# Optimization experiments

Hardware: AMD Instinct MI355X
Metric: run time of the kernel (lower is better)

Reference implementation:

```python
import jax, jax.numpy as jnp
import numpy as np

N = 100_000      # nodes
E = 1_600_000    # edges
DIN = 128
DH = 128
DOUT = 2
BN_EPS = 1e-5


def setup_inputs() -> dict:
    key = jax.random.key(0)
    ks = jax.random.split(key, 14)
    s_in = 1.0 / np.sqrt(DIN)
    s_h = 1.0 / np.sqrt(DH)
    return {
        "x": jax.random.normal(ks[0], (N, DIN), jnp.float32),
        "edge_index": jax.random.randint(ks[1], (2, E), 0, N, jnp.int32),
        "W1": jax.random.normal(ks[2], (DIN, DH), jnp.float32) * s_in,
        "b1": jnp.zeros((DH,), jnp.float32),
        "W2": jax.random.normal(ks[3], (DH, DH), jnp.float32) * s_h,
        "b2": jnp.zeros((DH,), jnp.float32),
        "W3": jax.random.normal(ks[4], (DH, DH), jnp.float32) * s_h,
        "b3": jnp.zeros((DH,), jnp.float32),
        "gamma": jnp.ones((DH,), jnp.float32),
        "beta": jnp.zeros((DH,), jnp.float32),
        "Wc": jax.random.normal(ks[5], (DH, DH), jnp.float32) * s_h,
        "bc": jnp.zeros((DH,), jnp.float32),
        "Wr": jax.random.normal(ks[6], (DH, DOUT), jnp.float32) * s_h,
        "br": jnp.zeros((DOUT,), jnp.float32),
    }


def reference(x, edge_index, W1, b1, W2, b2, W3, b3, gamma, beta, Wc, bc, Wr, br):
    src, dst = edge_index[0], edge_index[1]
    # GCN symmetric normalization with self-loops (deg includes self-loop)
    deg = jnp.zeros((N,), x.dtype).at[dst].add(1.0) + 1.0
    dinv = jax.lax.rsqrt(deg)
    coef = (dinv[src] * dinv[dst])[:, None]        # [E,1]
    self_coef = (dinv * dinv)[:, None]             # [N,1] self-loop weight

    def gcn_conv(h, W, b):
        h = h @ W                                  # [N,DH] dense transform
        agg = jnp.zeros((N, h.shape[1]), h.dtype).at[dst].add(h[src] * coef)
        return agg + h * self_coef + b

    h = jax.nn.relu(gcn_conv(x, W1, b1))
    h = jax.nn.relu(gcn_conv(h, W2, b2))   # dropout is identity at inference
    h = jax.nn.relu(gcn_conv(h, W3, b3))
    # BatchNorm1d over the node dimension (training-mode batch statistics)
    mu = h.mean(axis=0)
    var = h.var(axis=0)
    h = (h - mu) * jax.lax.rsqrt(var + BN_EPS) * gamma + beta
    h = jax.nn.relu(h @ Wc + bc)
    return h @ Wr + br
```

## Files before the change

### kernel.cpp

```cpp
#include <hip/hip_runtime.h>

#define DHC 128
#define BSHIFT 8
#define BSIZE 256

typedef __attribute__((ext_vector_type(8))) __bf16 bf16x8;
typedef __attribute__((ext_vector_type(8))) unsigned short ushort8;
typedef __attribute__((ext_vector_type(4))) float floatx4;

__device__ inline unsigned short f2bf(float f) {
    unsigned int u = __float_as_uint(f);
    return (unsigned short)((u + 0x7FFFu + ((u >> 16) & 1u)) >> 16);
}
__device__ inline float bf2f_lo(unsigned int v) { return __uint_as_float(v << 16); }
__device__ inline float bf2f_hi(unsigned int v) { return __uint_as_float(v & 0xFFFF0000u); }


__global__ __launch_bounds__(256) void bucket_hist(const int* __restrict__ dst,
                                                   int* __restrict__ bcount, int e) {
    __shared__ int h[512];
    for (int i = threadIdx.x; i < 512; i += 256) h[i] = 0;
    __syncthreads();
    int base = blockIdx.x * 4096 + threadIdx.x;
#pragma unroll
    for (int j = 0; j < 16; j++) {
        int i = base + j * 256;
        if (i < e) atomicAdd(&h[dst[i] >> BSHIFT], 1);
    }
    __syncthreads();
    for (int i = threadIdx.x; i < 512; i += 256)
        if (h[i]) atomicAdd(&bcount[i], h[i]);
}

__global__ void bucket_scan(const int* __restrict__ bcount, int* __restrict__ bbase,
                            int* __restrict__ bcur, int* __restrict__ row_ptr,
                            int nb, int n, int e) {
    __shared__ int s[512];
    int t = threadIdx.x;
    s[t] = (t < nb) ? bcount[t] : 0;
    __syncthreads();
    for (int off = 1; off < 512; off <<= 1) {
        int add = (t >= off) ? s[t - off] : 0;
        __syncthreads();
        s[t] += add;
        __syncthreads();
    }
    if (t < nb) {
        int ex = (t == 0) ? 0 : s[t - 1];
        bbase[t] = ex;
        bcur[t] = ex;
    }
    if (t == 0) {
        bbase[nb] = e;
        row_ptr[n] = e;
    }
}

__global__ __launch_bounds__(256) void bucket_scatter(const int* __restrict__ src,
                                                      const int* __restrict__ dst,
                                                      int* __restrict__ bcur,
                                                      unsigned int* __restrict__ ebuf, int e) {
    __shared__ int h[512];
    __shared__ int rsv[512];
    for (int i = threadIdx.x; i < 512; i += 256) h[i] = 0;
    __syncthreads();
    int base = blockIdx.x * 4096 + threadIdx.x;
    int sreg[16], dreg[16];
#pragma unroll
    for (int j = 0; j < 16; j++) {
        int i = base + j * 256;
        if (i < e) {
            sreg[j] = src[i];
            dreg[j] = dst[i];
            atomicAdd(&h[dreg[j] >> BSHIFT], 1);
        } else {
            dreg[j] = -1;
        }
    }
    __syncthreads();
    for (int i = threadIdx.x; i < 512; i += 256) {
        int c = h[i];
        rsv[i] = c ? atomicAdd(&bcur[i], c) : 0;
        h[i] = 0;
    }
    __syncthreads();
#pragma unroll
    for (int j = 0; j < 16; j++) {
        if (dreg[j] >= 0) {
            int b = dreg[j] >> BSHIFT;
            int pos = rsv[b] + atomicAdd(&h[b], 1);
            ebuf[pos] = (unsigned int)sreg[j] | ((unsigned int)(dreg[j] & (BSIZE - 1)) << 20);
        }
    }
}

__global__ __launch_bounds__(256) void bucket_build(const unsigned int* __restrict__ ebuf,
                                                    const int* __restrict__ bbase,
                                                    int* __restrict__ row_ptr,
                                                    int* __restrict__ csr_src,
                                                    float* __restrict__ dinv, int n) {
    __shared__ int ldeg[256];
    __shared__ int lcur[256];
    int b = blockIdx.x;
    int t = threadIdx.x;
    int beg = bbase[b], end = bbase[b + 1];
    ldeg[t] = 0;
    __syncthreads();
    for (int i = beg + t; i < end; i += 256) atomicAdd(&ldeg[ebuf[i] >> 20], 1);
    __syncthreads();
    int deg = ldeg[t];
    lcur[t] = deg;
    __syncthreads();
    for (int off = 1; off < 256; off <<= 1) {
        int add = (t >= off) ? lcur[t - off] : 0;
        __syncthreads();
        lcur[t] += add;
        __syncthreads();
    }
    int rp = beg + lcur[t] - deg;
    int node = (b << BSHIFT) + t;
    if (node < n) {
        row_ptr[node] = rp;
        dinv[node] = rsqrtf((float)(deg + 1));
    }
    __syncthreads();
    lcur[t] = rp;
    __syncthreads();
    for (int i = beg + t; i < end; i += 256) {
        unsigned int p = ebuf[i];
        int pos = atomicAdd(&lcur[p >> 20], 1);
        csr_src[pos] = (int)(p & 0xFFFFFu);
    }
}

__global__ void wconv3_k(const float* __restrict__ W1, const float* __restrict__ W2,
                         const float* __restrict__ W3, unsigned short* __restrict__ WTall) {
    int idx = blockIdx.x * 256 + threadIdx.x;
    int wsel = idx >> 14;
    int i = idx & 16383;
    int nn = i >> 7, k = i & 127;
    const float* W = (wsel == 0) ? W1 : (wsel == 1) ? W2 : W3;
    WTall[idx] = f2bf(W[k * 128 + nn]);
}

template <int MODE, int AF32>
__global__ __launch_bounds__(256, 4) void gemm_k(const void* __restrict__ Avoid,
                                                 const unsigned short* __restrict__ WT,
                                                 const float* __restrict__ bias,
                                                 unsigned short* __restrict__ outB,
                                                 float* __restrict__ outF,
                                                 const float* __restrict__ Wr,
                                                 const float* __restrict__ br, int n) {
    __shared__ unsigned short Ws[32 * 512];
    {
        for (int c = threadIdx.x; c < 2048; c += 256) {
            int f = c >> 6;
            int l = c & 63;
            int ks = f >> 3, ct = f & 7;
            int nn = ct * 16 + (l & 15);
            int kb = ks * 32 + (l >> 4) * 8;
            *(uint4*)(&Ws[c * 8]) = *(const uint4*)(&WT[nn * 128 + kb]);
        }
    }
    __syncthreads();
    const int wave = threadIdx.x >> 6;
    const int lane = threadIdx.x & 63;
    const int rowbase = blockIdx.x * 128 + wave * 32;
    const int m = lane & 15;
    const int kq = lane >> 4;

    floatx4 acc[2][8];
#pragma unroll
    for (int rt = 0; rt < 2; rt++)
#pragma unroll
        for (int ct = 0; ct < 8; ct++) acc[rt][ct] = (floatx4){0.f, 0.f, 0.f, 0.f};

    const int r0 = min(rowbase + m, n - 1);
    const int r1 = min(rowbase + 16 + m, n - 1);

#pragma unroll
    for (int ks = 0; ks < 4; ks++) {
        const int kb = ks * 32 + kq * 8;
        bf16x8 a0, a1;
        if (AF32) {
            const float* Af = (const float*)Avoid;
            float4 f00 = *(const float4*)(Af + (size_t)r0 * 128 + kb);
            float4 f01 = *(const float4*)(Af + (size_t)r0 * 128 + kb + 4);
            float4 f10 = *(const float4*)(Af + (size_t)r1 * 128 + kb);
            float4 f11 = *(const float4*)(Af + (size_t)r1 * 128 + kb + 4);
            ushort8 u0, u1;
            u0[0] = f2bf(f00.x); u0[1] = f2bf(f00.y); u0[2] = f2bf(f00.z); u0[3] = f2bf(f00.w);
            u0[4] = f2bf(f01.x); u0[5] = f2bf(f01.y); u0[6] = f2bf(f01.z); u0[7] = f2bf(f01.w);
            u1[0] = f2bf(f10.x); u1[1] = f2bf(f10.y); u1[2] = f2bf(f10.z); u1[3] = f2bf(f10.w);
            u1[4] = f2bf(f11.x); u1[5] = f2bf(f11.y); u1[6] = f2bf(f11.z); u1[7] = f2bf(f11.w);
            a0 = __builtin_bit_cast(bf16x8, u0);
            a1 = __builtin_bit_cast(bf16x8, u1);
        } else {
            const unsigned short* Ab = (const unsigned short*)Avoid;
            a0 = __builtin_bit_cast(bf16x8, *(const ushort8*)(Ab + (size_t)r0 * 128 + kb));
            a1 = __builtin_bit_cast(bf16x8, *(const ushort8*)(Ab + (size_t)r1 * 128 + kb));
        }
#pragma unroll
        for (int ct = 0; ct < 8; ct++) {
            bf16x8 bfr = __builtin_bit_cast(bf16x8,
                *(const ushort8*)(&Ws[(ks * 8 + ct) * 512 + lane * 8]));
            acc[0][ct] = __builtin_amdgcn_mfma_f32_16x16x32_bf16(a0, bfr, acc[0][ct], 0, 0, 0);
            acc[1][ct] = __builtin_amdgcn_mfma_f32_16x16x32_bf16(a1, bfr, acc[1][ct], 0, 0, 0);
        }
    }

    if (MODE == 0) {
#pragma unroll
        for (int rt = 0; rt < 2; rt++) {
#pragma unroll
            for (int ct = 0; ct < 8; ct++) {
                int col = ct * 16 + m;
#pragma unroll
                for (int i = 0; i < 4; i++) {
                    int r = rowbase + rt * 16 + kq * 4 + i;
                    if (r < n) outB[(size_t)r * 128 + col] = f2bf(acc[rt][ct][i]);
                }
            }
        }
    } else {
        float bcv[8], wr0[8], wr1[8];
#pragma unroll
        for (int ct = 0; ct < 8; ct++) {
            int col = ct * 16 + m;
            bcv[ct] = bias[col];
            float2 wv = ((const float2*)Wr)[col];
            wr0[ct] = wv.x;
            wr1[ct] = wv.y;
        }
        float br0 = br[0], br1 = br[1];
#pragma unroll
        for (int rt = 0; rt < 2; rt++) {
#pragma unroll
            for (int i = 0; i < 4; i++) {
                float p0 = 0.f, p1 = 0.f;
#pragma unroll
                for (int ct = 0; ct < 8; ct++) {
                    float v = fmaxf(acc[rt][ct][i] + bcv[ct], 0.f);
                    p0 = fmaf(v, wr0[ct], p0);
                    p1 = fmaf(v, wr1[ct], p1);
                }
#pragma unroll
                for (int mk = 1; mk < 16; mk <<= 1) {
                    p0 += __shfl_xor(p0, mk);
                    p1 += __shfl_xor(p1, mk);
                }
                int r = rowbase + rt * 16 + kq * 4 + i;
                if (m == 0 && r < n) ((float2*)outF)[r] = make_float2(p0 + br0, p1 + br1);
            }
        }
    }
}

__global__ __launch_bounds__(256) void agg_k(const unsigned short* __restrict__ hW,
                                             const int* __restrict__ csr,
                                             const int* __restrict__ row_ptr,
                                             const float* __restrict__ dinv,
                                             const float* __restrict__ bias,
                                             unsigned short* __restrict__ out, int n) {
    int node = blockIdx.x * 16 + (threadIdx.x >> 4);
    int t = threadIdx.x & 15;
    if (node >= n) return;
    int beg = row_ptr[node], end = row_ptr[node + 1];
    float dd = dinv[node];
    const uint4* h4 = (const uint4*)hW;
    float a[8];
#pragma unroll
    for (int i = 0; i < 8; i++) a[i] = 0.f;

    int e = beg;
    for (; e + 3 < end; e += 4) {
        int s0 = csr[e + 0], s1 = csr[e + 1], s2 = csr[e + 2], s3 = csr[e + 3];
        float c0 = dinv[s0] * dd, c1 = dinv[s1] * dd, c2 = dinv[s2] * dd, c3 = dinv[s3] * dd;
        uint4 v0 = h4[(size_t)s0 * 16 + t];
        uint4 v1 = h4[(size_t)s1 * 16 + t];
        uint4 v2 = h4[(size_t)s2 * 16 + t];
        uint4 v3 = h4[(size_t)s3 * 16 + t];
        a[0] = fmaf(c0, bf2f_lo(v0.x), a[0]); a[1] = fmaf(c0, bf2f_hi(v0.x), a[1]);
        a[2] = fmaf(c0, bf2f_lo(v0.y), a[2]); a[3] = fmaf(c0, bf2f_hi(v0.y), a[3]);
        a[4] = fmaf(c0, bf2f_lo(v0.z), a[4]); a[5] = fmaf(c0, bf2f_hi(v0.z), a[5]);
        a[6] = fmaf(c0, bf2f_lo(v0.w), a[6]); a[7] = fmaf(c0, bf2f_hi(v0.w), a[7]);
        a[0] = fmaf(c1, bf2f_lo(v1.x), a[0]); a[1] = fmaf(c1, bf2f_hi(v1.x), a[1]);
        a[2] = fmaf(c1, bf2f_lo(v1.y), a[2]); a[3] = fmaf(c1, bf2f_hi(v1.y), a[3]);
        a[4] = fmaf(c1, bf2f_lo(v1.z), a[4]); a[5] = fmaf(c1, bf2f_hi(v1.z), a[5]);
        a[6] = fmaf(c1, bf2f_lo(v1.w), a[6]); a[7] = fmaf(c1, bf2f_hi(v1.w), a[7]);
        a[0] = fmaf(c2, bf2f_lo(v2.x), a[0]); a[1] = fmaf(c2, bf2f_hi(v2.x), a[1]);
        a[2] = fmaf(c2, bf2f_lo(v2.y), a[2]); a[3] = fmaf(c2, bf2f_hi(v2.y), a[3]);
        a[4] = fmaf(c2, bf2f_lo(v2.z), a[4]); a[5] = fmaf(c2, bf2f_hi(v2.z), a[5]);
        a[6] = fmaf(c2, bf2f_lo(v2.w), a[6]); a[7] = fmaf(c2, bf2f_hi(v2.w), a[7]);
        a[0] = fmaf(c3, bf2f_lo(v3.x), a[0]); a[1] = fmaf(c3, bf2f_hi(v3.x), a[1]);
        a[2] = fmaf(c3, bf2f_lo(v3.y), a[2]); a[3] = fmaf(c3, bf2f_hi(v3.y), a[3]);
        a[4] = fmaf(c3, bf2f_lo(v3.z), a[4]); a[5] = fmaf(c3, bf2f_hi(v3.z), a[5]);
        a[6] = fmaf(c3, bf2f_lo(v3.w), a[6]); a[7] = fmaf(c3, bf2f_hi(v3.w), a[7]);
    }
    for (; e < end; e++) {
        int s = csr[e];
        float c = dinv[s] * dd;
        uint4 v = h4[(size_t)s * 16 + t];
        a[0] = fmaf(c, bf2f_lo(v.x), a[0]); a[1] = fmaf(c, bf2f_hi(v.x), a[1]);
        a[2] = fmaf(c, bf2f_lo(v.y), a[2]); a[3] = fmaf(c, bf2f_hi(v.y), a[3]);
        a[4] = fmaf(c, bf2f_lo(v.z), a[4]); a[5] = fmaf(c, bf2f_hi(v.z), a[5]);
        a[6] = fmaf(c, bf2f_lo(v.w), a[6]); a[7] = fmaf(c, bf2f_hi(v.w), a[7]);
    }

    {
        float sc = dd * dd;
        uint4 v = h4[(size_t)node * 16 + t];
        a[0] = fmaf(sc, bf2f_lo(v.x), a[0]); a[1] = fmaf(sc, bf2f_hi(v.x), a[1]);
        a[2] = fmaf(sc, bf2f_lo(v.y), a[2]); a[3] = fmaf(sc, bf2f_hi(v.y), a[3]);
        a[4] = fmaf(sc, bf2f_lo(v.z), a[4]); a[5] = fmaf(sc, bf2f_hi(v.z), a[5]);
        a[6] = fmaf(sc, bf2f_lo(v.w), a[6]); a[7] = fmaf(sc, bf2f_hi(v.w), a[7]);
    }
    float4 b0 = ((const float4*)bias)[t * 2];
    float4 b1 = ((const float4*)bias)[t * 2 + 1];
    uint4 o;
    o.x = (unsigned int)f2bf(fmaxf(a[0] + b0.x, 0.f)) |
          ((unsigned int)f2bf(fmaxf(a[1] + b0.y, 0.f)) << 16);
    o.y = (unsigned int)f2bf(fmaxf(a[2] + b0.z, 0.f)) |
          ((unsigned int)f2bf(fmaxf(a[3] + b0.w, 0.f)) << 16);
    o.z = (unsigned int)f2bf(fmaxf(a[4] + b1.x, 0.f)) |
          ((unsigned int)f2bf(fmaxf(a[5] + b1.y, 0.f)) << 16);
    o.w = (unsigned int)f2bf(fmaxf(a[6] + b1.z, 0.f)) |
          ((unsigned int)f2bf(fmaxf(a[7] + b1.w, 0.f)) << 16);
    ((uint4*)out)[(size_t)node * 16 + t] = o;
}

__global__ __launch_bounds__(256) void bn_stats(const unsigned short* __restrict__ h,
                                                float* __restrict__ gsum,
                                                float* __restrict__ gsumsq, int n) {
    __shared__ float red[4][256];
    int l = threadIdx.x & 63;
    int rs = threadIdx.x >> 6;
    float s0 = 0.f, s1 = 0.f, q0 = 0.f, q1 = 0.f;
    for (int r = blockIdx.x * 4 + rs; r < n; r += gridDim.x * 4) {
        unsigned int v = *(const unsigned int*)(h + (size_t)r * 128 + l * 2);
        float a = bf2f_lo(v), b = bf2f_hi(v);
        s0 += a;
        s1 += b;
        q0 = fmaf(a, a, q0);
        q1 = fmaf(b, b, q1);
    }
    red[0][threadIdx.x] = s0;
    red[1][threadIdx.x] = s1;
    red[2][threadIdx.x] = q0;
    red[3][threadIdx.x] = q1;
    __syncthreads();
    if (threadIdx.x < 64) {
        float S0 = 0.f, S1 = 0.f, Q0 = 0.f, Q1 = 0.f;
#pragma unroll
        for (int j = 0; j < 4; j++) {
            S0 += red[0][j * 64 + l];
            S1 += red[1][j * 64 + l];
            Q0 += red[2][j * 64 + l];
            Q1 += red[3][j * 64 + l];
        }
        atomicAdd(&gsum[2 * l + 0], S0);
        atomicAdd(&gsum[2 * l + 1], S1);
        atomicAdd(&gsumsq[2 * l + 0], Q0);
        atomicAdd(&gsumsq[2 * l + 1], Q1);
    }
}

__global__ void bn_finalize(const float* __restrict__ gsum, const float* __restrict__ gsumsq,
                            const float* __restrict__ gamma, const float* __restrict__ beta,
                            const float* __restrict__ bc, float* __restrict__ scale,
                            float* __restrict__ shift, float* __restrict__ bcP, float invN) {
    int j = threadIdx.x;
    float mu = gsum[j] * invN;
    float var = gsumsq[j] * invN - mu * mu;
    float sc = gamma[j] * rsqrtf(var + 1e-5f);
    scale[j] = sc;
    shift[j] = beta[j] - mu * sc;
    bcP[j] = bc[j];
}

__global__ __launch_bounds__(256) void wcfold(const float* __restrict__ Wc,
                                              const float* __restrict__ scale,
                                              const float* __restrict__ shift,
                                              unsigned short* __restrict__ WcT,
                                              float* __restrict__ bcP) {
    __shared__ float scS[128], shS[128];
    if (threadIdx.x < 128) {
        scS[threadIdx.x] = scale[threadIdx.x];
        shS[threadIdx.x] = shift[threadIdx.x];
    }
    __syncthreads();
    int idx = blockIdx.x * 256 + threadIdx.x;
    int j = idx & 127, k = idx >> 7;
    float w = Wc[k * 128 + j];
    WcT[j * 128 + k] = f2bf(scS[k] * w);
    atomicAdd(&bcP[j], shS[k] * w);
}


extern "C" void kernel_launch(void* const* d_in, const int* in_sizes, int n_in,
                              void* d_out, int out_size, void* d_ws, size_t ws_size,
                              hipStream_t stream) {
    const float* x = (const float*)d_in[0];
    const int* ei = (const int*)d_in[1];
    const float* W1 = (const float*)d_in[2];
    const float* b1 = (const float*)d_in[3];
    const float* W2 = (const float*)d_in[4];
    const float* b2 = (const float*)d_in[5];
    const float* W3 = (const float*)d_in[6];
    const float* b3 = (const float*)d_in[7];
    const float* gamma = (const float*)d_in[8];
    const float* beta = (const float*)d_in[9];
    const float* Wc = (const float*)d_in[10];
    const float* bc = (const float*)d_in[11];
    const float* Wr = (const float*)d_in[12];
    const float* br = (const float*)d_in[13];
    float* out = (float*)d_out;

    const int N = in_sizes[0] / DHC;
    const int E = in_sizes[1] / 2;
    const int* srcIdx = ei;
    const int* dstIdx = ei + E;
    const int NB = (N + BSIZE - 1) >> BSHIFT;

    char* w = (char*)d_ws;
    size_t off = 0;
    auto alloc = [&](size_t bytes) -> void* {
        void* p = w + off;
        off += (bytes + 255) & ~(size_t)255;
        return p;
    };
    unsigned short* bufA = (unsigned short*)alloc((size_t)N * DHC * 2);
    unsigned short* bufB = (unsigned short*)alloc((size_t)N * DHC * 2);
    unsigned int* ebuf = (unsigned int*)alloc((size_t)E * 4);
    int* csr_src = (int*)alloc((size_t)E * 4);
    int* row_ptr = (int*)alloc((size_t)(N + 1) * 4);
    float* dinv = (float*)alloc((size_t)N * 4);
    int* bcount = (int*)alloc(512 * 4 + 256 * 4);
    float* stats = (float*)(bcount + 512);
    float* gsum = stats;
    float* gsumsq = stats + 128;
    int* bbase = (int*)alloc(512 * 4);
    int* bcur = (int*)alloc(512 * 4);
    unsigned short* WTall = (unsigned short*)alloc((size_t)3 * 16384 * 2);
    unsigned short* WT1 = WTall;
    unsigned short* WT2 = WTall + 16384;
    unsigned short* WT3 = WTall + 32768;
    unsigned short* WcT = (unsigned short*)alloc(16384 * 2);
    float* scale = (float*)alloc(128 * 4);
    float* shift = (float*)alloc(128 * 4);
    float* bcP = (float*)alloc(128 * 4);
    (void)ws_size; (void)n_in; (void)out_size;

    hipMemsetAsync(bcount, 0, 512 * 4 + 256 * 4, stream);

    const int EB = (E + 4095) / 4096;
    bucket_hist<<<EB, 256, 0, stream>>>(dstIdx, bcount, E);
    bucket_scan<<<1, 512, 0, stream>>>(bcount, bbase, bcur, row_ptr, NB, N, E);
    bucket_scatter<<<EB, 256, 0, stream>>>(srcIdx, dstIdx, bcur, ebuf, E);
    bucket_build<<<NB, 256, 0, stream>>>(ebuf, bbase, row_ptr, csr_src, dinv, N);

    wconv3_k<<<192, 256, 0, stream>>>(W1, W2, W3, WTall);

    const int gemmBlocks = (N + 127) / 128;
    const int aggBlocks = (N + 15) / 16;

    gemm_k<0, 1><<<gemmBlocks, 256, 0, stream>>>(x, WT1, nullptr, bufB, nullptr, nullptr, nullptr, N);
    agg_k<<<aggBlocks, 256, 0, stream>>>(bufB, csr_src, row_ptr, dinv, b1, bufA, N);
    gemm_k<0, 0><<<gemmBlocks, 256, 0, stream>>>(bufA, WT2, nullptr, bufB, nullptr, nullptr, nullptr, N);
    agg_k<<<aggBlocks, 256, 0, stream>>>(bufB, csr_src, row_ptr, dinv, b2, bufA, N);
    gemm_k<0, 0><<<gemmBlocks, 256, 0, stream>>>(bufA, WT3, nullptr, bufB, nullptr, nullptr, nullptr, N);
    agg_k<<<aggBlocks, 256, 0, stream>>>(bufB, csr_src, row_ptr, dinv, b3, bufA, N);

    bn_stats<<<256, 256, 0, stream>>>(bufA, gsum, gsumsq, N);
    bn_finalize<<<1, 128, 0, stream>>>(gsum, gsumsq, gamma, beta, bc, scale, shift, bcP, 1.0f / (float)N);
    wcfold<<<64, 256, 0, stream>>>(Wc, scale, shift, WcT, bcP);
    gemm_k<2, 0><<<gemmBlocks, 256, 0, stream>>>(bufA, WcT, bcP, nullptr, out, Wr, br, N);
}
```

Baseline: 449.0 us.

## Prescale GEMM output by dinv and pad CSR rows to 8 for branchless aggregation

The GEMM epilogue now multiplies each output row by dinv[row], so aggregation only sums neighbor rows and applies the destination dinv once, dropping the per-edge dinv gather and multiply. CSR rows are padded to multiples of 8 with a dummy zero row at index N, which lets agg_k load indices as int4 pairs, prefetch the next group, and run an 8-wide unrolled loop with no tail. Building this CSR takes an extra degree pass and a second scan kernel. Padding adds up to seven dummy gathers per node, and rounding to bf16 after prescaling changes numerics slightly.

```diff
diff --git a/kernel.cpp b/kernel.cpp
--- a/kernel.cpp
+++ b/kernel.cpp
@@ -33,8 +33,7 @@
 }
 
 __global__ void bucket_scan(const int* __restrict__ bcount, int* __restrict__ bbase,
-                            int* __restrict__ bcur, int* __restrict__ row_ptr,
-                            int nb, int n, int e) {
+                            int* __restrict__ bcur, int nb, int e) {
     __shared__ int s[512];
     int t = threadIdx.x;
     s[t] = (t < nb) ? bcount[t] : 0;
@@ -50,10 +49,7 @@
         bbase[t] = ex;
         bcur[t] = ex;
     }
-    if (t == 0) {
-        bbase[nb] = e;
-        row_ptr[n] = e;
-    }
+    if (t == 0) bbase[nb] = e;
 }
 
 __global__ __launch_bounds__(256) void bucket_scatter(const int* __restrict__ src,
@@ -94,47 +90,97 @@
     }
 }
 
-__global__ __launch_bounds__(256) void bucket_build(const unsigned int* __restrict__ ebuf,
-                                                    const int* __restrict__ bbase,
-                                                    int* __restrict__ row_ptr,
-                                                    int* __restrict__ csr_src,
-                                                    float* __restrict__ dinv, int n) {
+__global__ __launch_bounds__(256) void bucket_dega(const unsigned int* __restrict__ ebuf,
+                                                   const int* __restrict__ bbase,
+                                                   int* __restrict__ degs,
+                                                   int* __restrict__ pbsum,
+                                                   float* __restrict__ dinv, int n) {
     __shared__ int ldeg[256];
-    __shared__ int lcur[256];
-    int b = blockIdx.x;
-    int t = threadIdx.x;
+    __shared__ int red[256];
+    int b = blockIdx.x, t = threadIdx.x;
     int beg = bbase[b], end = bbase[b + 1];
     ldeg[t] = 0;
     __syncthreads();
     for (int i = beg + t; i < end; i += 256) atomicAdd(&ldeg[ebuf[i] >> 20], 1);
     __syncthreads();
+    int node = (b << BSHIFT) + t;
     int deg = ldeg[t];
-    lcur[t] = deg;
+    int pdeg = (deg + 7) & ~7;
+    if (node < n) {
+        degs[node] = deg;
+        dinv[node] = rsqrtf((float)(deg + 1));
+    } else {
+        pdeg = 0;
+    }
+    red[t] = pdeg;
+    __syncthreads();
+    for (int off = 128; off > 0; off >>= 1) {
+        if (t < off) red[t] += red[t + off];
+        __syncthreads();
+    }
+    if (t == 0) pbsum[b] = red[0];
+}
+
+__global__ void pscan(const int* __restrict__ pbsum, int* __restrict__ pbase,
+                      int* __restrict__ row_ptr, int nb, int n) {
+    __shared__ int s[512];
+    int t = threadIdx.x;
+    s[t] = (t < nb) ? pbsum[t] : 0;
+    __syncthreads();
+    for (int off = 1; off < 512; off <<= 1) {
+        int add = (t >= off) ? s[t - off] : 0;
+        __syncthreads();
+        s[t] += add;
+        __syncthreads();
+    }
+    if (t < nb) pbase[t] = (t == 0) ? 0 : s[t - 1];
+    if (t == 0) {
+        pbase[nb] = s[nb - 1];
+        row_ptr[n] = s[nb - 1];
+    }
+}
+
+__global__ __launch_bounds__(256) void bucket_csr(const unsigned int* __restrict__ ebuf,
+                                                  const int* __restrict__ bbase,
+                                                  const int* __restrict__ pbase,
+                                                  const int* __restrict__ degs,
+                                                  int* __restrict__ row_ptr,
+                                                  int* __restrict__ csr, int n) {
+    __shared__ int lcur[256];
+    __shared__ int lscan[256];
+    int b = blockIdx.x, t = threadIdx.x;
+    int beg = bbase[b], end = bbase[b + 1];
+    int node = (b << BSHIFT) + t;
+    int deg = (node < n) ? degs[node] : 0;
+    int pdeg = (deg + 7) & ~7;
+    lscan[t] = pdeg;
     __syncthreads();
     for (int off = 1; off < 256; off <<= 1) {
-        int add = (t >= off) ? lcur[t - off] : 0;
-        __syncthreads();
-        lcur[t] += add;
-        __syncthreads();
-    }
-    int rp = beg + lcur[t] - deg;
-    int node = (b << BSHIFT) + t;
-    if (node < n) {
-        row_ptr[node] = rp;
-        dinv[node] = rsqrtf((float)(deg + 1));
-    }
-    __syncthreads();
+        int add = (t >= off) ? lscan[t - off] : 0;
+        __syncthreads();
+        lscan[t] += add;
+        __syncthreads();
+    }
+    int rp = pbase[b] + lscan[t] - pdeg;
+    if (node < n) row_ptr[node] = rp;
     lcur[t] = rp;
     __syncthreads();
     for (int i = beg + t; i < end; i += 256) {
         unsigned int p = ebuf[i];
         int pos = atomicAdd(&lcur[p >> 20], 1);
-        csr_src[pos] = (int)(p & 0xFFFFFu);
-    }
+        csr[pos] = (int)(p & 0xFFFFFu);
+    }
+    __syncthreads();
+    for (int j = deg; j < pdeg; j++) csr[rp + j] = n;
 }
 
 __global__ void wconv3_k(const float* __restrict__ W1, const float* __restrict__ W2,
-                         const float* __restrict__ W3, unsigned short* __restrict__ WTall) {
+                         const float* __restrict__ W3, unsigned short* __restrict__ WTall,
+                         unsigned short* __restrict__ dumA, unsigned short* __restrict__ dumB) {
+    if (blockIdx.x == 0 && threadIdx.x < 128) {
+        dumA[threadIdx.x] = 0;
+        dumB[threadIdx.x] = 0;
+    }
     int idx = blockIdx.x * 256 + threadIdx.x;
     int wsel = idx >> 14;
     int i = idx & 16383;
@@ -150,7 +196,8 @@
                                                  unsigned short* __restrict__ outB,
                                                  float* __restrict__ outF,
                                                  const float* __restrict__ Wr,
-                                                 const float* __restrict__ br, int n) {
+                                                 const float* __restrict__ br,
+                                                 const float* __restrict__ dinvp, int n) {
     __shared__ unsigned short Ws[32 * 512];
     {
         for (int c = threadIdx.x; c < 2048; c += 256) {
@@ -213,12 +260,15 @@
 #pragma unroll
         for (int rt = 0; rt < 2; rt++) {
 #pragma unroll
-            for (int ct = 0; ct < 8; ct++) {
-                int col = ct * 16 + m;
-#pragma unroll
-                for (int i = 0; i < 4; i++) {
-                    int r = rowbase + rt * 16 + kq * 4 + i;
-                    if (r < n) outB[(size_t)r * 128 + col] = f2bf(acc[rt][ct][i]);
+            for (int i = 0; i < 4; i++) {
+                int r = rowbase + rt * 16 + kq * 4 + i;
+                if (r < n) {
+                    float dv = dinvp[r];
+#pragma unroll
+                    for (int ct = 0; ct < 8; ct++) {
+                        int col = ct * 16 + m;
+                        outB[(size_t)r * 128 + col] = f2bf(acc[rt][ct][i] * dv);
+                    }
                 }
             }
         }
@@ -256,7 +306,13 @@
     }
 }
 
-__global__ __launch_bounds__(256) void agg_k(const unsigned short* __restrict__ hW,
+#define ACC8(v)                                          \
+    a[0] += bf2f_lo((v).x); a[1] += bf2f_hi((v).x);      \
+    a[2] += bf2f_lo((v).y); a[3] += bf2f_hi((v).y);      \
+    a[4] += bf2f_lo((v).z); a[5] += bf2f_hi((v).z);      \
+    a[6] += bf2f_lo((v).w); a[7] += bf2f_hi((v).w);
+
+__global__ __launch_bounds__(256) void agg_k(const unsigned short* __restrict__ hS,
                                              const int* __restrict__ csr,
                                              const int* __restrict__ row_ptr,
                                              const float* __restrict__ dinv,
@@ -265,67 +321,49 @@
     int node = blockIdx.x * 16 + (threadIdx.x >> 4);
     int t = threadIdx.x & 15;
     if (node >= n) return;
-    int beg = row_ptr[node], end = row_ptr[node + 1];
+    const uint4* h4 = (const uint4*)hS;
+    uint4 vs = h4[(size_t)node * 16 + t];
+    int beg = row_ptr[node], pend = row_ptr[node + 1];
     float dd = dinv[node];
-    const uint4* h4 = (const uint4*)hW;
+
     float a[8];
-#pragma unroll
-    for (int i = 0; i < 8; i++) a[i] = 0.f;
-
-    int e = beg;
-    for (; e + 3 < end; e += 4) {
-        int s0 = csr[e + 0], s1 = csr[e + 1], s2 = csr[e + 2], s3 = csr[e + 3];
-        float c0 = dinv[s0] * dd, c1 = dinv[s1] * dd, c2 = dinv[s2] * dd, c3 = dinv[s3] * dd;
-        uint4 v0 = h4[(size_t)s0 * 16 + t];
-        uint4 v1 = h4[(size_t)s1 * 16 + t];
-        uint4 v2 = h4[(size_t)s2 * 16 + t];
-        uint4 v3 = h4[(size_t)s3 * 16 + t];
-        a[0] = fmaf(c0, bf2f_lo(v0.x), a[0]); a[1] = fmaf(c0, bf2f_hi(v0.x), a[1]);
-        a[2] = fmaf(c0, bf2f_lo(v0.y), a[2]); a[3] = fmaf(c0, bf2f_hi(v0.y), a[3]);
-        a[4] = fmaf(c0, bf2f_lo(v0.z), a[4]); a[5] = fmaf(c0, bf2f_hi(v0.z), a[5]);
-        a[6] = fmaf(c0, bf2f_lo(v0.w), a[6]); a[7] = fmaf(c0, bf2f_hi(v0.w), a[7]);
-        a[0] = fmaf(c1, bf2f_lo(v1.x), a[0]); a[1] = fmaf(c1, bf2f_hi(v1.x), a[1]);
-        a[2] = fmaf(c1, bf2f_lo(v1.y), a[2]); a[3] = fmaf(c1, bf2f_hi(v1.y), a[3]);
-        a[4] = fmaf(c1, bf2f_lo(v1.z), a[4]); a[5] = fmaf(c1, bf2f_hi(v1.z), a[5]);
-        a[6] = fmaf(c1, bf2f_lo(v1.w), a[6]); a[7] = fmaf(c1, bf2f_hi(v1.w), a[7]);
-        a[0] = fmaf(c2, bf2f_lo(v2.x), a[0]); a[1] = fmaf(c2, bf2f_hi(v2.x), a[1]);
-        a[2] = fmaf(c2, bf2f_lo(v2.y), a[2]); a[3] = fmaf(c2, bf2f_hi(v2.y), a[3]);
-        a[4] = fmaf(c2, bf2f_lo(v2.z), a[4]); a[5] = fmaf(c2, bf2f_hi(v2.z), a[5]);
-        a[6] = fmaf(c2, bf2f_lo(v2.w), a[6]); a[7] = fmaf(c2, bf2f_hi(v2.w), a[7]);
-        a[0] = fmaf(c3, bf2f_lo(v3.x), a[0]); a[1] = fmaf(c3, bf2f_hi(v3.x), a[1]);
-        a[2] = fmaf(c3, bf2f_lo(v3.y), a[2]); a[3] = fmaf(c3, bf2f_hi(v3.y), a[3]);
-        a[4] = fmaf(c3, bf2f_lo(v3.z), a[4]); a[5] = fmaf(c3, bf2f_hi(v3.z), a[5]);
-        a[6] = fmaf(c3, bf2f_lo(v3.w), a[6]); a[7] = fmaf(c3, bf2f_hi(v3.w), a[7]);
-    }
-    for (; e < end; e++) {
-        int s = csr[e];
-        float c = dinv[s] * dd;
-        uint4 v = h4[(size_t)s * 16 + t];
-        a[0] = fmaf(c, bf2f_lo(v.x), a[0]); a[1] = fmaf(c, bf2f_hi(v.x), a[1]);
-        a[2] = fmaf(c, bf2f_lo(v.y), a[2]); a[3] = fmaf(c, bf2f_hi(v.y), a[3]);
-        a[4] = fmaf(c, bf2f_lo(v.z), a[4]); a[5] = fmaf(c, bf2f_hi(v.z), a[5]);
-        a[6] = fmaf(c, bf2f_lo(v.w), a[6]); a[7] = fmaf(c, bf2f_hi(v.w), a[7]);
-    }
-
-    {
-        float sc = dd * dd;
-        uint4 v = h4[(size_t)node * 16 + t];
-        a[0] = fmaf(sc, bf2f_lo(v.x), a[0]); a[1] = fmaf(sc, bf2f_hi(v.x), a[1]);
-        a[2] = fmaf(sc, bf2f_lo(v.y), a[2]); a[3] = fmaf(sc, bf2f_hi(v.y), a[3]);
-        a[4] = fmaf(sc, bf2f_lo(v.z), a[4]); a[5] = fmaf(sc, bf2f_hi(v.z), a[5]);
-        a[6] = fmaf(sc, bf2f_lo(v.w), a[6]); a[7] = fmaf(sc, bf2f_hi(v.w), a[7]);
-    }
+    a[0] = bf2f_lo(vs.x); a[1] = bf2f_hi(vs.x);
+    a[2] = bf2f_lo(vs.y); a[3] = bf2f_hi(vs.y);
+    a[4] = bf2f_lo(vs.z); a[5] = bf2f_hi(vs.z);
+    a[6] = bf2f_lo(vs.w); a[7] = bf2f_hi(vs.w);
+
+    const int4* cp = (const int4*)(csr + beg);
+    int nc = (pend - beg) >> 3;
+    if (nc > 0) {
+        int4 i0 = cp[0], i1 = cp[1];
+        for (int k = 0; k < nc; k++) {
+            uint4 v0 = h4[(size_t)(unsigned)i0.x * 16 + t];
+            uint4 v1 = h4[(size_t)(unsigned)i0.y * 16 + t];
+            uint4 v2 = h4[(size_t)(unsigned)i0.z * 16 + t];
+            uint4 v3 = h4[(size_t)(unsigned)i0.w * 16 + t];
+            uint4 v4 = h4[(size_t)(unsigned)i1.x * 16 + t];
+            uint4 v5 = h4[(size_t)(unsigned)i1.y * 16 + t];
+            uint4 v6 = h4[(size_t)(unsigned)i1.z * 16 + t];
+            uint4 v7 = h4[(size_t)(unsigned)i1.w * 16 + t];
+            int4 p0 = cp[2 * k + 2];
+            int4 p1 = cp[2 * k + 3];
+            ACC8(v0); ACC8(v1); ACC8(v2); ACC8(v3);
+            ACC8(v4); ACC8(v5); ACC8(v6); ACC8(v7);
+            i0 = p0; i1 = p1;
+        }
+    }
+
     float4 b0 = ((const float4*)bias)[t * 2];
     float4 b1 = ((const float4*)bias)[t * 2 + 1];
     uint4 o;
-    o.x = (unsigned int)f2bf(fmaxf(a[0] + b0.x, 0.f)) |
-          ((unsigned int)f2bf(fmaxf(a[1] + b0.y, 0.f)) << 16);
-    o.y = (unsigned int)f2bf(fmaxf(a[2] + b0.z, 0.f)) |
-          ((unsigned int)f2bf(fmaxf(a[3] + b0.w, 0.f)) << 16);
-    o.z = (unsigned int)f2bf(fmaxf(a[4] + b1.x, 0.f)) |
-          ((unsigned int)f2bf(fmaxf(a[5] + b1.y, 0.f)) << 16);
-    o.w = (unsigned int)f2bf(fmaxf(a[6] + b1.z, 0.f)) |
-          ((unsigned int)f2bf(fmaxf(a[7] + b1.w, 0.f)) << 16);
+    o.x = (unsigned int)f2bf(fmaxf(fmaf(dd, a[0], b0.x), 0.f)) |
+          ((unsigned int)f2bf(fmaxf(fmaf(dd, a[1], b0.y), 0.f)) << 16);
+    o.y = (unsigned int)f2bf(fmaxf(fmaf(dd, a[2], b0.z), 0.f)) |
+          ((unsigned int)f2bf(fmaxf(fmaf(dd, a[3], b0.w), 0.f)) << 16);
+    o.z = (unsigned int)f2bf(fmaxf(fmaf(dd, a[4], b1.x), 0.f)) |
+          ((unsigned int)f2bf(fmaxf(fmaf(dd, a[5], b1.y), 0.f)) << 16);
+    o.w = (unsigned int)f2bf(fmaxf(fmaf(dd, a[6], b1.z), 0.f)) |
+          ((unsigned int)f2bf(fmaxf(fmaf(dd, a[7], b1.w), 0.f)) << 16);
     ((uint4*)out)[(size_t)node * 16 + t] = o;
 }
 
@@ -429,18 +467,21 @@
         off += (bytes + 255) & ~(size_t)255;
         return p;
     };
-    unsigned short* bufA = (unsigned short*)alloc((size_t)N * DHC * 2);
-    unsigned short* bufB = (unsigned short*)alloc((size_t)N * DHC * 2);
+    unsigned short* bufA = (unsigned short*)alloc((size_t)(N + 1) * DHC * 2);
+    unsigned short* bufB = (unsigned short*)alloc((size_t)(N + 1) * DHC * 2);
     unsigned int* ebuf = (unsigned int*)alloc((size_t)E * 4);
-    int* csr_src = (int*)alloc((size_t)E * 4);
+    int* csr_src = (int*)alloc(((size_t)E + 8 * (size_t)N + 16) * 4);
     int* row_ptr = (int*)alloc((size_t)(N + 1) * 4);
     float* dinv = (float*)alloc((size_t)N * 4);
+    int* degs = (int*)alloc((size_t)N * 4);
     int* bcount = (int*)alloc(512 * 4 + 256 * 4);
     float* stats = (float*)(bcount + 512);
     float* gsum = stats;
     float* gsumsq = stats + 128;
-    int* bbase = (int*)alloc(512 * 4);
+    int* bbase = (int*)alloc(513 * 4);
     int* bcur = (int*)alloc(512 * 4);
+    int* pbsum = (int*)alloc(512 * 4);
+    int* pbase = (int*)alloc(513 * 4);
     unsigned short* WTall = (unsigned short*)alloc((size_t)3 * 16384 * 2);
     unsigned short* WT1 = WTall;
     unsigned short* WT2 = WTall + 16384;
@@ -455,24 +496,27 @@
 
     const int EB = (E + 4095) / 4096;
     bucket_hist<<<EB, 256, 0, stream>>>(dstIdx, bcount, E);
-    bucket_scan<<<1, 512, 0, stream>>>(bcount, bbase, bcur, row_ptr, NB, N, E);
+    bucket_scan<<<1, 512, 0, stream>>>(bcount, bbase, bcur, NB, E);
     bucket_scatter<<<EB, 256, 0, stream>>>(srcIdx, dstIdx, bcur, ebuf, E);
-    bucket_build<<<NB, 256, 0, stream>>>(ebuf, bbase, row_ptr, csr_src, dinv, N);
-
-    wconv3_k<<<192, 256, 0, stream>>>(W1, W2, W3, WTall);
+    bucket_dega<<<NB, 256, 0, stream>>>(ebuf, bbase, degs, pbsum, dinv, N);
+    pscan<<<1, 512, 0, stream>>>(pbsum, pbase, row_ptr, NB, N);
+    bucket_csr<<<NB, 256, 0, stream>>>(ebuf, bbase, pbase, degs, row_ptr, csr_src, N);
+
+    wconv3_k<<<192, 256, 0, stream>>>(W1, W2, W3, WTall,
+                                      bufA + (size_t)N * DHC, bufB + (size_t)N * DHC);
 
     const int gemmBlocks = (N + 127) / 128;
     const int aggBlocks = (N + 15) / 16;
 
-    gemm_k<0, 1><<<gemmBlocks, 256, 0, stream>>>(x, WT1, nullptr, bufB, nullptr, nullptr, nullptr, N);
+    gemm_k<0, 1><<<gemmBlocks, 256, 0, stream>>>(x, WT1, nullptr, bufB, nullptr, nullptr, nullptr, dinv, N);
     agg_k<<<aggBlocks, 256, 0, stream>>>(bufB, csr_src, row_ptr, dinv, b1, bufA, N);
-    gemm_k<0, 0><<<gemmBlocks, 256, 0, stream>>>(bufA, WT2, nullptr, bufB, nullptr, nullptr, nullptr, N);
+    gemm_k<0, 0><<<gemmBlocks, 256, 0, stream>>>(bufA, WT2, nullptr, bufB, nullptr, nullptr, nullptr, dinv, N);
     agg_k<<<aggBlocks, 256, 0, stream>>>(bufB, csr_src, row_ptr, dinv, b2, bufA, N);
-    gemm_k<0, 0><<<gemmBlocks, 256, 0, stream>>>(bufA, WT3, nullptr, bufB, nullptr, nullptr, nullptr, N);
+    gemm_k<0, 0><<<gemmBlocks, 256, 0, stream>>>(bufA, WT3, nullptr, bufB, nullptr, nullptr, nullptr, dinv, N);
     agg_k<<<aggBlocks, 256, 0, stream>>>(bufB, csr_src, row_ptr, dinv, b3, bufA, N);
 
     bn_stats<<<256, 256, 0, stream>>>(bufA, gsum, gsumsq, N);
     bn_finalize<<<1, 128, 0, stream>>>(gsum, gsumsq, gamma, beta, bc, scale, shift, bcP, 1.0f / (float)N);
     wcfold<<<64, 256, 0, stream>>>(Wc, scale, shift, WcT, bcP);
-    gemm_k<2, 0><<<gemmBlocks, 256, 0, stream>>>(bufA, WcT, bcP, nullptr, out, Wr, br, N);
-}
+    gemm_k<2, 0><<<gemmBlocks, 256, 0, stream>>>(bufA, WcT, bcP, nullptr, out, Wr, br, dinv, N);
+}
```

Measured after the change: 449.9 us (median of 2 runs). About the same (+0.2%).
